# Kernel optimization log

Hardware: AMD Instinct MI355X
Metric: run time of the kernel (lower is better)

## Reference

```python
import jax, jax.numpy as jnp
import numpy as np

CROP_H = 14
CROP_W = 14
EXTRAPOLATION_VALUE = 0.0


def setup_inputs() -> dict:
    key = jax.random.key(0)
    k1, k2, k3 = jax.random.split(key, 3)
    image = jax.random.normal(k1, (8, 256, 100, 152), dtype=jnp.float32)
    # normalized box coords in [0,1]; (y1,x1,y2,x2), y2<y1 allowed (extrapolation handles it)
    boxes = jax.random.uniform(k2, (1000, 4), dtype=jnp.float32)
    box_ind = jax.random.randint(k3, (1000,), 0, 8, dtype=jnp.int32)
    return {"image": image, "boxes": boxes, "box_ind": box_ind}


def _crop_and_resize(image, boxes, box_ind):
    # image: [B, C, H, W]; boxes: [N, 4] (y1, x1, y2, x2) normalized; box_ind: [N]
    B, C, H, W = image.shape
    dt = image.dtype
    y1, x1, y2, x2 = boxes[:, 0], boxes[:, 1], boxes[:, 2], boxes[:, 3]

    # TF crop_and_resize sampling grid (crop size > 1 path)
    h_scale = (y2 - y1) * (H - 1) / (CROP_H - 1)          # [N]
    w_scale = (x2 - x1) * (W - 1) / (CROP_W - 1)          # [N]
    in_y = y1[:, None] * (H - 1) + jnp.arange(CROP_H, dtype=dt)[None, :] * h_scale[:, None]  # [N, ch]
    in_x = x1[:, None] * (W - 1) + jnp.arange(CROP_W, dtype=dt)[None, :] * w_scale[:, None]  # [N, cw]

    valid_y = (in_y >= 0) & (in_y <= H - 1)               # [N, ch]
    valid_x = (in_x >= 0) & (in_x <= W - 1)               # [N, cw]

    top = jnp.floor(in_y)
    left = jnp.floor(in_x)
    y_lerp = in_y - top                                    # [N, ch]
    x_lerp = in_x - left                                   # [N, cw]

    ti = jnp.clip(top, 0, H - 1).astype(jnp.int32)         # top index    [N, ch]
    bi = jnp.clip(top + 1, 0, H - 1).astype(jnp.int32)     # bottom index [N, ch]
    li = jnp.clip(left, 0, W - 1).astype(jnp.int32)        # left index   [N, cw]
    ri = jnp.clip(left + 1, 0, W - 1).astype(jnp.int32)    # right index  [N, cw]

    b = box_ind[:, None, None]                             # [N, 1, 1]
    yt = ti[:, :, None]
    yb = bi[:, :, None]
    xl = li[:, None, :]
    xr = ri[:, None, :]

    # mixed advanced indexing -> gathered dims first: [N, ch, cw, C]
    tl = image[b, :, yt, xl]
    tr = image[b, :, yt, xr]
    bl = image[b, :, yb, xl]
    br = image[b, :, yb, xr]

    xw = x_lerp[:, None, :, None]                          # [N, 1, cw, 1]
    yw = y_lerp[:, :, None, None]                          # [N, ch, 1, 1]
    top_v = tl + (tr - tl) * xw
    bot_v = bl + (br - bl) * xw
    val = top_v + (bot_v - top_v) * yw                     # [N, ch, cw, C]

    valid = (valid_y[:, :, None] & valid_x[:, None, :])[..., None]
    out = jnp.where(valid, val, jnp.asarray(EXTRAPOLATION_VALUE, dt))
    return jnp.transpose(out, (0, 3, 1, 2))                # [N, C, ch, cw]


def reference(image, boxes, box_ind):
    return _crop_and_resize(image, boxes, box_ind)
```

## Files before the change

kernel.cpp:

```cpp
#include <hip/hip_runtime.h>

#define CROP_H 14
#define CROP_W 14
#define IMG_B 8
#define IMG_C 256
#define IMG_H 100
#define IMG_W 152
#define NBOX 1000
#define PLANE (IMG_H * IMG_W)
#define ZOFF  PLANE
#define POS (CROP_H * CROP_W)
#define PAIRS (POS / 2)
#define OUT_PER_BOX (IMG_C * POS)
#define BOXCAP 64
#define CG 32
#define NCG (IMG_C / CG)

typedef float f2u __attribute__((ext_vector_type(2), aligned(8)));
typedef float f4u __attribute__((ext_vector_type(4), aligned(16)));

__global__ __launch_bounds__(1024) void sort_boxes_kernel(
    const int* __restrict__ box_ind,
    int* __restrict__ perm,
    int* __restrict__ offsets)
{
    __shared__ unsigned s_mask[IMG_B][32];
    __shared__ int s_tot[IMG_B];
    const int tid = threadIdx.x;

    if (tid < IMG_B * 32) ((unsigned*)s_mask)[tid] = 0u;
    __syncthreads();

    int key = 0;
    if (tid < NBOX) {
        key = box_ind[tid];
        atomicOr(&s_mask[key][tid >> 5], 1u << (tid & 31));
    }
    __syncthreads();

    if (tid < IMG_B) {
        int t = 0;
        #pragma unroll
        for (int w = 0; w < 32; ++w) t += __popc(s_mask[tid][w]);
        s_tot[tid] = t;
    }
    __syncthreads();

    if (tid == 0) {
        int acc = 0;
        #pragma unroll
        for (int k = 0; k < IMG_B; ++k) { offsets[k] = acc; acc += s_tot[k]; }
        offsets[IMG_B] = acc;
    }

    if (tid < NBOX) {
        int base = 0;
        #pragma unroll
        for (int k = 0; k < IMG_B; ++k) base += (k < key) ? s_tot[k] : 0;
        const int w = tid >> 5, b = tid & 31;
        int r = __popc(s_mask[key][w] & ((b == 0) ? 0u : ((1u << b) - 1u)));
        for (int ww = 0; ww < w; ++ww) r += __popc(s_mask[key][ww]);
        perm[base + r] = tid;
    }
}

__global__ __launch_bounds__(1024, 8) void CropAndResize_16630113370849_kernel(
    const float* __restrict__ image,
    const float* __restrict__ boxes,
    const int* __restrict__ perm,
    const int* __restrict__ offsets,
    float* __restrict__ out)
{
    __shared__ __align__(16) float s_plane[15360];
    __shared__ f2u s_row[BOXCAP * CROP_H];
    __shared__ f4u s_colp[BOXCAP * 7];
    __shared__ unsigned s_ob[BOXCAP];

    const int c   = blockIdx.x;
    const int b   = blockIdx.y;
    const int tid = threadIdx.x;

    {
        const float4* __restrict__ src =
            (const float4*)(image + ((size_t)b * IMG_C + c) * PLANE);
        float4* dst = (float4*)s_plane;
        #pragma unroll
        for (int i = 0; i < 4; ++i) {
            const int e = i * 1024 + tid;
            if (e < PLANE / 4) dst[e] = src[e];
        }
        if (tid < 160) s_plane[ZOFF + tid] = 0.0f;
    }

    const int s0 = offsets[b], s1 = offsets[b + 1];
    const unsigned cPOS = (unsigned)(c * POS);

    for (int ck = s0; ck < s1; ck += BOXCAP) {
        const int cnt = min(BOXCAP, s1 - ck);

        __syncthreads();

        for (int j = tid; j < cnt * 21; j += 1024) {
            const int slot = j / 21;
            const int t    = j - slot * 21;
            const int n    = perm[ck + slot];
            if (t == 0) s_ob[slot] = (unsigned)(n * OUT_PER_BOX);

            const float y1 = boxes[n * 4 + 0];
            const float x1 = boxes[n * 4 + 1];
            const float y2 = boxes[n * 4 + 2];
            const float x2 = boxes[n * 4 + 3];

            if (t < CROP_H) {
                const float hs   = __fdiv_rn(__fmul_rn(__fsub_rn(y2, y1), (float)(IMG_H - 1)),
                                             (float)(CROP_H - 1));
                const float in_y = __fadd_rn(__fmul_rn(y1, (float)(IMG_H - 1)),
                                             __fmul_rn((float)t, hs));
                const int vy = (in_y >= 0.0f) && (in_y <= (float)(IMG_H - 1));
                const float top = floorf(in_y);
                const float yw  = __fsub_rn(in_y, top);
                const int ti = (int)fminf(fmaxf(top, 0.0f), (float)(IMG_H - 1));
                const int r0 = min(ti, IMG_H - 2);
                const bool sely = (ti == IMG_H - 1);
                f2u e;
                e.x = __int_as_float(vy ? (r0 * IMG_W) : ZOFF);
                e.y = sely ? 1.0f : yw;
                s_row[slot * CROP_H + t] = e;
            } else {
                const int xg = t - CROP_H;
                const float ws = __fdiv_rn(__fmul_rn(__fsub_rn(x2, x1), (float)(IMG_W - 1)),
                                           (float)(CROP_W - 1));
                const float x1W = __fmul_rn(x1, (float)(IMG_W - 1));
                f4u e;
                #pragma unroll
                for (int k = 0; k < 2; ++k) {
                    const int x = 2 * xg + k;
                    const float in_x = __fadd_rn(x1W, __fmul_rn((float)x, ws));
                    const int vx = (in_x >= 0.0f) && (in_x <= (float)(IMG_W - 1));
                    const float left = floorf(in_x);
                    const float xw   = __fsub_rn(in_x, left);
                    const int li = (int)fminf(fmaxf(left, 0.0f), (float)(IMG_W - 1));
                    const int c0 = min(li, IMG_W - 2);
                    const bool selx = (li == IMG_W - 1);
                    const int   cb  = vx ? c0 : ZOFF;
                    const float xwp = selx ? 1.0f : xw;
                    if (k == 0) { e.x = __int_as_float(cb); e.y = xwp; }
                    else        { e.z = __int_as_float(cb); e.w = xwp; }
                }
                s_colp[slot * 7 + xg] = e;
            }
        }
        __syncthreads();

        const int total = cnt * PAIRS;
        #pragma unroll 2
        for (int q = tid; q < total; q += 1024) {
            const int slot = q / PAIRS;
            const int rem  = q - slot * PAIRS;
            const int y    = rem / 7;
            const int xg   = rem - y * 7;

            const f2u re = s_row[slot * CROP_H + y];
            const f4u ce = s_colp[slot * 7 + xg];
            const int   rb  = __float_as_int(re.x);
            const float yw  = re.y;
            const int   cb0 = __float_as_int(ce.x);
            const float xw0 = ce.y;
            const int   cb1 = __float_as_int(ce.z);
            const float xw1 = ce.w;

            const int off0 = min(rb + cb0, ZOFF);
            const int off1 = min(rb + cb1, ZOFF);

            const float* __restrict__ p0 = s_plane + off0;
            const float* __restrict__ p1 = s_plane + off1;

            const float a0 = p0[0], a1 = p0[1];
            const float b0 = p0[IMG_W], b1 = p0[IMG_W + 1];
            const float t0 = a0 + (a1 - a0) * xw0;
            const float u0 = b0 + (b1 - b0) * xw0;
            const float v0 = t0 + (u0 - t0) * yw;

            const float c0_ = p1[0], c1_ = p1[1];
            const float d0_ = p1[IMG_W], d1_ = p1[IMG_W + 1];
            const float t1 = c0_ + (c1_ - c0_) * xw1;
            const float u1 = d0_ + (d1_ - d0_) * xw1;
            const float v1 = t1 + (u1 - t1) * yw;

            f2u res; res.x = v0; res.y = v1;
            *(f2u*)(out + (size_t)(s_ob[slot] + cPOS + (unsigned)(2 * rem))) = res;
        }
    }
}

__global__ __launch_bounds__(256) void crop_chw_kernel(
    const float* __restrict__ image,
    const float* __restrict__ boxes,
    const int* __restrict__ box_ind,
    float* __restrict__ out)
{
    const int bid  = blockIdx.x;
    const int cg   = bid & 7;
    const int n    = bid >> 3;
    const int tid  = threadIdx.x;
    if (tid >= POS) return;

    const int b = box_ind[n];
    const int y = tid / CROP_W;
    const int x = tid - y * CROP_W;

    const float y1 = boxes[n * 4 + 0];
    const float x1 = boxes[n * 4 + 1];
    const float y2 = boxes[n * 4 + 2];
    const float x2 = boxes[n * 4 + 3];

    const float hs   = __fdiv_rn(__fmul_rn(__fsub_rn(y2, y1), (float)(IMG_H - 1)),
                                 (float)(CROP_H - 1));
    const float in_y = __fadd_rn(__fmul_rn(y1, (float)(IMG_H - 1)),
                                 __fmul_rn((float)y, hs));
    const int vy = (in_y >= 0.0f) && (in_y <= (float)(IMG_H - 1));
    const float top = floorf(in_y);
    const float yw  = __fsub_rn(in_y, top);
    const int ti = (int)fminf(fmaxf(top, 0.0f), (float)(IMG_H - 1));

    const float ws   = __fdiv_rn(__fmul_rn(__fsub_rn(x2, x1), (float)(IMG_W - 1)),
                                 (float)(CROP_W - 1));
    const float in_x = __fadd_rn(__fmul_rn(x1, (float)(IMG_W - 1)),
                                 __fmul_rn((float)x, ws));
    const int vx = (in_x >= 0.0f) && (in_x <= (float)(IMG_W - 1));
    const float left = floorf(in_x);
    const float xw   = __fsub_rn(in_x, left);
    const int li = (int)fminf(fmaxf(left, 0.0f), (float)(IMG_W - 1));

    const int r0 = min(ti, IMG_H - 2);
    const int c0 = min(li, IMG_W - 2);
    const bool sely = (ti == IMG_H - 1);
    const bool selx = (li == IMG_W - 1);
    const bool vald = (vy & vx) != 0;

    const float* __restrict__ pl =
        image + (size_t)b * (size_t)(IMG_C * PLANE)
              + (size_t)(cg * CG) * PLANE + (r0 * IMG_W + c0);
    float* __restrict__ po =
        out + (size_t)n * (size_t)OUT_PER_BOX + (size_t)(cg * CG) * POS + tid;

    #pragma unroll 8
    for (int cl = 0; cl < CG; ++cl) {
        const float2 ra = *(const float2*)(pl);
        const float2 rb = *(const float2*)(pl + IMG_W);
        const float tA = sely ? rb.x : ra.x;
        const float tB = sely ? rb.y : ra.y;
        const float tl = selx ? tB : tA;
        const float bl = selx ? rb.y : rb.x;
        const float top_v = __fadd_rn(tl, __fmul_rn(__fsub_rn(tB, tl), xw));
        const float bot_v = __fadd_rn(bl, __fmul_rn(__fsub_rn(rb.y, bl), xw));
        const float v = __fadd_rn(top_v, __fmul_rn(__fsub_rn(bot_v, top_v), yw));
        *po = vald ? v : 0.0f;
        pl += PLANE;
        po += POS;
    }
}

extern "C" void kernel_launch(void* const* d_in, const int* in_sizes, int n_in,
                              void* d_out, int out_size, void* d_ws, size_t ws_size,
                              hipStream_t stream) {
    const float* image  = (const float*)d_in[0];
    const float* boxes  = (const float*)d_in[1];
    const int*   boxind = (const int*)d_in[2];
    float* out = (float*)d_out;

    const size_t need = (NBOX + IMG_B + 1) * sizeof(int);
    if (ws_size >= need) {
        int* perm    = (int*)d_ws;
        int* offsets = perm + NBOX;

        sort_boxes_kernel<<<1, 1024, 0, stream>>>(boxind, perm, offsets);
        CropAndResize_16630113370849_kernel<<<dim3(IMG_C, IMG_B), 1024, 0, stream>>>(
            image, boxes, perm, offsets, out);
    } else {
        crop_chw_kernel<<<dim3(NBOX * NCG), 256, 0, stream>>>(
            image, boxes, boxind, out);
    }
}
```

Measured before the change: 98.73 us.

## Precompute per-box sampling tables in a separate kernel and remap threads per box

Moves the per-box row/column sampling computation out of the main kernel, which repeated it in every (channel, batch) block, into a separate build_packs kernel. That kernel writes packed tables to workspace in sorted order, and the main kernel just copies them into shared memory. The box chunk size drops from 64 to 16, and each of 16 wavefronts now owns one box, handling two fixed pairs per thread with no divisions. This adds a kernel launch and a larger workspace requirement, and needs more chunk iterations and barriers per block.

```diff
diff --git a/kernel.cpp b/kernel.cpp
--- a/kernel.cpp
+++ b/kernel.cpp
@@ -12,12 +12,19 @@
 #define POS (CROP_H * CROP_W)
 #define PAIRS (POS / 2)
 #define OUT_PER_BOX (IMG_C * POS)
-#define BOXCAP 64
+#define BOXCAP 16
 #define CG 32
 #define NCG (IMG_C / CG)
 
 typedef float f2u __attribute__((ext_vector_type(2), aligned(8)));
 typedef float f4u __attribute__((ext_vector_type(4), aligned(16)));
+
+#define WS_ROWG   0
+#define WS_COLG   112000
+#define WS_OBOX   224000
+#define WS_PERM   228000
+#define WS_OFFS   232000
+#define WS_NEED   232036
 
 __global__ __launch_bounds__(1024) void sort_boxes_kernel(
     const int* __restrict__ box_ind,
@@ -64,17 +71,77 @@
     }
 }
 
+__global__ __launch_bounds__(64) void build_packs_kernel(
+    const float* __restrict__ boxes,
+    const int* __restrict__ perm,
+    f2u* __restrict__ rowG,
+    f4u* __restrict__ colG,
+    unsigned* __restrict__ oboxG)
+{
+    const int s = blockIdx.x;
+    const int t = threadIdx.x;
+    if (t >= 22) return;
+    const int n = perm[s];
+
+    if (t == 21) { oboxG[s] = (unsigned)(n * OUT_PER_BOX); return; }
+
+    const float y1 = boxes[n * 4 + 0];
+    const float x1 = boxes[n * 4 + 1];
+    const float y2 = boxes[n * 4 + 2];
+    const float x2 = boxes[n * 4 + 3];
+
+    if (t < CROP_H) {
+        const float hs   = __fdiv_rn(__fmul_rn(__fsub_rn(y2, y1), (float)(IMG_H - 1)),
+                                     (float)(CROP_H - 1));
+        const float in_y = __fadd_rn(__fmul_rn(y1, (float)(IMG_H - 1)),
+                                     __fmul_rn((float)t, hs));
+        const int vy = (in_y >= 0.0f) && (in_y <= (float)(IMG_H - 1));
+        const float top = floorf(in_y);
+        const float yw  = __fsub_rn(in_y, top);
+        const int ti = (int)fminf(fmaxf(top, 0.0f), (float)(IMG_H - 1));
+        const int r0 = min(ti, IMG_H - 2);
+        const bool sely = (ti == IMG_H - 1);
+        f2u e;
+        e.x = __int_as_float(vy ? (r0 * IMG_W) : ZOFF);
+        e.y = sely ? 1.0f : yw;
+        rowG[s * CROP_H + t] = e;
+    } else {
+        const int xg = t - CROP_H;
+        const float ws = __fdiv_rn(__fmul_rn(__fsub_rn(x2, x1), (float)(IMG_W - 1)),
+                                   (float)(CROP_W - 1));
+        const float x1W = __fmul_rn(x1, (float)(IMG_W - 1));
+        f4u e;
+        #pragma unroll
+        for (int k = 0; k < 2; ++k) {
+            const int x = 2 * xg + k;
+            const float in_x = __fadd_rn(x1W, __fmul_rn((float)x, ws));
+            const int vx = (in_x >= 0.0f) && (in_x <= (float)(IMG_W - 1));
+            const float left = floorf(in_x);
+            const float xw   = __fsub_rn(in_x, left);
+            const int li = (int)fminf(fmaxf(left, 0.0f), (float)(IMG_W - 1));
+            const int c0 = min(li, IMG_W - 2);
+            const bool selx = (li == IMG_W - 1);
+            const int   cb  = vx ? c0 : ZOFF;
+            const float xwp = selx ? 1.0f : xw;
+            if (k == 0) { e.x = __int_as_float(cb); e.y = xwp; }
+            else        { e.z = __int_as_float(cb); e.w = xwp; }
+        }
+        colG[s * 7 + xg] = e;
+    }
+}
+
 __global__ __launch_bounds__(1024, 8) void CropAndResize_16630113370849_kernel(
     const float* __restrict__ image,
-    const float* __restrict__ boxes,
-    const int* __restrict__ perm,
+    const f2u* __restrict__ rowG,
+    const f4u* __restrict__ colG,
+    const unsigned* __restrict__ oboxG,
     const int* __restrict__ offsets,
     float* __restrict__ out)
 {
     __shared__ __align__(16) float s_plane[15360];
     __shared__ f2u s_row[BOXCAP * CROP_H];
     __shared__ f4u s_colp[BOXCAP * 7];
-    __shared__ unsigned s_ob[BOXCAP];
+    __shared__ unsigned s_obox[BOXCAP];
 
     const int c   = blockIdx.x;
     const int b   = blockIdx.y;
@@ -92,103 +159,87 @@
         if (tid < 160) s_plane[ZOFF + tid] = 0.0f;
     }
 
-    const int s0 = offsets[b], s1 = offsets[b + 1];
+    const int slot = tid >> 6;
+    const int r0   = tid & 63;
+    const int r1   = r0 + 64;
+    const int y0   = (r0 * 9363) >> 16;
+    const int xg0  = r0 - y0 * 7;
+    const int y1i  = (r1 * 9363) >> 16;
+    const int xg1  = r1 - y1i * 7;
+    const bool has1 = (r1 < PAIRS);
+
+    const int s0 = offsets[b], nb = offsets[b + 1] - s0;
     const unsigned cPOS = (unsigned)(c * POS);
 
-    for (int ck = s0; ck < s1; ck += BOXCAP) {
-        const int cnt = min(BOXCAP, s1 - ck);
+    for (int ckb = 0; ckb < nb; ckb += BOXCAP) {
+        const int base = s0 + ckb;
+        const int cnt  = min(BOXCAP, nb - ckb);
 
         __syncthreads();
 
-        for (int j = tid; j < cnt * 21; j += 1024) {
-            const int slot = j / 21;
-            const int t    = j - slot * 21;
-            const int n    = perm[ck + slot];
-            if (t == 0) s_ob[slot] = (unsigned)(n * OUT_PER_BOX);
-
-            const float y1 = boxes[n * 4 + 0];
-            const float x1 = boxes[n * 4 + 1];
-            const float y2 = boxes[n * 4 + 2];
-            const float x2 = boxes[n * 4 + 3];
-
-            if (t < CROP_H) {
-                const float hs   = __fdiv_rn(__fmul_rn(__fsub_rn(y2, y1), (float)(IMG_H - 1)),
-                                             (float)(CROP_H - 1));
-                const float in_y = __fadd_rn(__fmul_rn(y1, (float)(IMG_H - 1)),
-                                             __fmul_rn((float)t, hs));
-                const int vy = (in_y >= 0.0f) && (in_y <= (float)(IMG_H - 1));
-                const float top = floorf(in_y);
-                const float yw  = __fsub_rn(in_y, top);
-                const int ti = (int)fminf(fmaxf(top, 0.0f), (float)(IMG_H - 1));
-                const int r0 = min(ti, IMG_H - 2);
-                const bool sely = (ti == IMG_H - 1);
-                f2u e;
-                e.x = __int_as_float(vy ? (r0 * IMG_W) : ZOFF);
-                e.y = sely ? 1.0f : yw;
-                s_row[slot * CROP_H + t] = e;
-            } else {
-                const int xg = t - CROP_H;
-                const float ws = __fdiv_rn(__fmul_rn(__fsub_rn(x2, x1), (float)(IMG_W - 1)),
-                                           (float)(CROP_W - 1));
-                const float x1W = __fmul_rn(x1, (float)(IMG_W - 1));
-                f4u e;
-                #pragma unroll
-                for (int k = 0; k < 2; ++k) {
-                    const int x = 2 * xg + k;
-                    const float in_x = __fadd_rn(x1W, __fmul_rn((float)x, ws));
-                    const int vx = (in_x >= 0.0f) && (in_x <= (float)(IMG_W - 1));
-                    const float left = floorf(in_x);
-                    const float xw   = __fsub_rn(in_x, left);
-                    const int li = (int)fminf(fmaxf(left, 0.0f), (float)(IMG_W - 1));
-                    const int c0 = min(li, IMG_W - 2);
-                    const bool selx = (li == IMG_W - 1);
-                    const int   cb  = vx ? c0 : ZOFF;
-                    const float xwp = selx ? 1.0f : xw;
-                    if (k == 0) { e.x = __int_as_float(cb); e.y = xwp; }
-                    else        { e.z = __int_as_float(cb); e.w = xwp; }
-                }
-                s_colp[slot * 7 + xg] = e;
-            }
+        if (tid < cnt * CROP_H) {
+            s_row[tid] = rowG[base * CROP_H + tid];
+        } else if (tid >= 256 && tid < 256 + cnt * 7) {
+            s_colp[tid - 256] = colG[base * 7 + (tid - 256)];
+        } else if (tid >= 384 && tid < 384 + cnt) {
+            s_obox[tid - 384] = oboxG[base + tid - 384];
         }
         __syncthreads();
 
-        const int total = cnt * PAIRS;
-        #pragma unroll 2
-        for (int q = tid; q < total; q += 1024) {
-            const int slot = q / PAIRS;
-            const int rem  = q - slot * PAIRS;
-            const int y    = rem / 7;
-            const int xg   = rem - y * 7;
-
-            const f2u re = s_row[slot * CROP_H + y];
-            const f4u ce = s_colp[slot * 7 + xg];
-            const int   rb  = __float_as_int(re.x);
-            const float yw  = re.y;
-            const int   cb0 = __float_as_int(ce.x);
-            const float xw0 = ce.y;
-            const int   cb1 = __float_as_int(ce.z);
-            const float xw1 = ce.w;
-
-            const int off0 = min(rb + cb0, ZOFF);
-            const int off1 = min(rb + cb1, ZOFF);
-
-            const float* __restrict__ p0 = s_plane + off0;
-            const float* __restrict__ p1 = s_plane + off1;
-
-            const float a0 = p0[0], a1 = p0[1];
-            const float b0 = p0[IMG_W], b1 = p0[IMG_W + 1];
-            const float t0 = a0 + (a1 - a0) * xw0;
-            const float u0 = b0 + (b1 - b0) * xw0;
-            const float v0 = t0 + (u0 - t0) * yw;
-
-            const float c0_ = p1[0], c1_ = p1[1];
-            const float d0_ = p1[IMG_W], d1_ = p1[IMG_W + 1];
-            const float t1 = c0_ + (c1_ - c0_) * xw1;
-            const float u1 = d0_ + (d1_ - d0_) * xw1;
-            const float v1 = t1 + (u1 - t1) * yw;
-
-            f2u res; res.x = v0; res.y = v1;
-            *(f2u*)(out + (size_t)(s_ob[slot] + cPOS + (unsigned)(2 * rem))) = res;
+        if (slot < cnt) {
+            const unsigned obase = s_obox[slot] + cPOS;
+            float* __restrict__ po = out + (size_t)obase;
+
+            {
+                const f2u re = s_row[slot * CROP_H + y0];
+                const f4u ce = s_colp[slot * 7 + xg0];
+                const int   rb  = __float_as_int(re.x);
+                const float yw  = re.y;
+                const int off0 = min(rb + __float_as_int(ce.x), ZOFF);
+                const int off1 = min(rb + __float_as_int(ce.z), ZOFF);
+                const float xw0 = ce.y, xw1 = ce.w;
+
+                const float* p0 = s_plane + off0;
+                const float* p1 = s_plane + off1;
+                const float a0 = p0[0], a1 = p0[1];
+                const float b0 = p0[IMG_W], b1 = p0[IMG_W + 1];
+                const float c0_ = p1[0], c1_ = p1[1];
+                const float d0_ = p1[IMG_W], d1_ = p1[IMG_W + 1];
+
+                const float t0 = a0 + (a1 - a0) * xw0;
+                const float u0 = b0 + (b1 - b0) * xw0;
+                const float t1 = c0_ + (c1_ - c0_) * xw1;
+                const float u1 = d0_ + (d1_ - d0_) * xw1;
+                f2u res;
+                res.x = t0 + (u0 - t0) * yw;
+                res.y = t1 + (u1 - t1) * yw;
+                *(f2u*)(po + 2 * r0) = res;
+            }
+            if (has1) {
+                const f2u re = s_row[slot * CROP_H + y1i];
+                const f4u ce = s_colp[slot * 7 + xg1];
+                const int   rb  = __float_as_int(re.x);
+                const float yw  = re.y;
+                const int off0 = min(rb + __float_as_int(ce.x), ZOFF);
+                const int off1 = min(rb + __float_as_int(ce.z), ZOFF);
+                const float xw0 = ce.y, xw1 = ce.w;
+
+                const float* p0 = s_plane + off0;
+                const float* p1 = s_plane + off1;
+                const float a0 = p0[0], a1 = p0[1];
+                const float b0 = p0[IMG_W], b1 = p0[IMG_W + 1];
+                const float c0_ = p1[0], c1_ = p1[1];
+                const float d0_ = p1[IMG_W], d1_ = p1[IMG_W + 1];
+
+                const float t0 = a0 + (a1 - a0) * xw0;
+                const float u0 = b0 + (b1 - b0) * xw0;
+                const float t1 = c0_ + (c1_ - c0_) * xw1;
+                const float u1 = d0_ + (d1_ - d0_) * xw1;
+                f2u res;
+                res.x = t0 + (u0 - t0) * yw;
+                res.y = t1 + (u1 - t1) * yw;
+                *(f2u*)(po + 2 * r1) = res;
+            }
         }
     }
 }
@@ -269,14 +320,18 @@
     const int*   boxind = (const int*)d_in[2];
     float* out = (float*)d_out;
 
-    const size_t need = (NBOX + IMG_B + 1) * sizeof(int);
-    if (ws_size >= need) {
-        int* perm    = (int*)d_ws;
-        int* offsets = perm + NBOX;
+    if (ws_size >= (size_t)WS_NEED) {
+        char* ws = (char*)d_ws;
+        f2u*      rowG    = (f2u*)(ws + WS_ROWG);
+        f4u*      colG    = (f4u*)(ws + WS_COLG);
+        unsigned* oboxG   = (unsigned*)(ws + WS_OBOX);
+        int*      perm    = (int*)(ws + WS_PERM);
+        int*      offsets = (int*)(ws + WS_OFFS);
 
         sort_boxes_kernel<<<1, 1024, 0, stream>>>(boxind, perm, offsets);
+        build_packs_kernel<<<NBOX, 64, 0, stream>>>(boxes, perm, rowG, colG, oboxG);
         CropAndResize_16630113370849_kernel<<<dim3(IMG_C, IMG_B), 1024, 0, stream>>>(
-            image, boxes, perm, offsets, out);
+            image, rowG, colG, oboxG, offsets, out);
     } else {
         crop_chw_kernel<<<dim3(NBOX * NCG), 256, 0, stream>>>(
             image, boxes, boxind, out);
```

Result: slower. 100.7 us (+2.0%).
